# Kernel optimization log

Hardware: AMD Instinct MI355X
Metric: run time of the kernel (lower is better)

## Reference

```python
import jax, jax.numpy as jnp
import numpy as np

N_NODES = 100000
N_EDGES = 1600000
FEAT = 128


def setup_inputs() -> dict:
    key = jax.random.key(0)
    k_h, k_hin, k_src, k_dst, k_w, k_b = jax.random.split(key, 6)
    h = jax.random.normal(k_h, (N_NODES, FEAT), dtype=jnp.float32)
    h_in = jax.random.normal(k_hin, (N_NODES, FEAT), dtype=jnp.float32)
    src = jax.random.randint(k_src, (N_EDGES,), 0, N_NODES, dtype=jnp.int64)
    dst = jax.random.randint(k_dst, (N_EDGES,), 0, N_NODES, dtype=jnp.int64)
    W = jax.random.normal(k_w, (FEAT, FEAT), dtype=jnp.float32) / np.sqrt(FEAT)
    b = jax.random.normal(k_b, (FEAT,), dtype=jnp.float32) * 0.01
    return {"h": h, "h_in": h_in, "src": src, "dst": dst, "W": W, "b": b}


def reference(h, h_in, src, dst, W, b):
    # h_in is accepted but unused, matching the original forward signature.
    n = h.shape[0]
    hr = jax.nn.relu(h @ W.T + b)  # [N, d]
    # copy_src message + mean reduce over in-edges == segment mean by dst
    msg_sum = jax.ops.segment_sum(hr[src], dst, num_segments=n)  # [N, d]
    deg = jax.ops.segment_sum(jnp.ones(dst.shape, dtype=hr.dtype), dst, num_segments=n)  # [N]
    agg = msg_sum / jnp.maximum(deg, 1.0)[:, None]
    # DGL UDF reduce only overwrites nodes with in-degree > 0;
    # zero-in-degree nodes keep their pre-aggregation feature hr.
    return jnp.where(deg[:, None] > 0, agg, hr)
```

## Files before the change

kernel.cpp:

```cpp
#include <hip/hip_runtime.h>
#include <hip/hip_bf16.h>


#define FEAT 128
#define BM 64
#define NPB 256
#define CAP 6144

using bf16 = __hip_bfloat16;
typedef __attribute__((ext_vector_type(8))) short short8_;
typedef __attribute__((ext_vector_type(4))) short bhalf4;
typedef __attribute__((ext_vector_type(4))) float floatx4;

__device__ __forceinline__ bhalf4 cvt4(float4 f) {
    bhalf4 s;
    s[0] = __bfloat16_as_short(__float2bfloat16(f.x));
    s[1] = __bfloat16_as_short(__float2bfloat16(f.y));
    s[2] = __bfloat16_as_short(__float2bfloat16(f.z));
    s[3] = __bfloat16_as_short(__float2bfloat16(f.w));
    return s;
}
__device__ __forceinline__ float b2f(short s) {
    return __bfloat162float(__short_as_bfloat16(s));
}

__launch_bounds__(256)
__global__ void gemm_kernel(const float* __restrict__ h, const float* __restrict__ W,
                            const float* __restrict__ b, bf16* __restrict__ hr, int M) {
    __shared__ bf16 sA[BM][136];
    __shared__ bf16 sW[FEAT][136];

    const int tid  = threadIdx.x;
    const int row0 = blockIdx.x * BM;

    #pragma unroll
    for (int i = 0; i < 8; ++i) {
        int v = i * 256 + tid;
        int r = v >> 4;
        int c = (v & 15) * 8;
        const float4* wp = (const float4*)(W + (size_t)r * FEAT + c);
        bhalf4 lo = cvt4(wp[0]);
        bhalf4 hi = cvt4(wp[1]);
        short8_ s;
        s[0] = lo[0]; s[1] = lo[1]; s[2] = lo[2]; s[3] = lo[3];
        s[4] = hi[0]; s[5] = hi[1]; s[6] = hi[2]; s[7] = hi[3];
        *(short8_*)(&sW[r][c]) = s;
    }
    #pragma unroll
    for (int i = 0; i < 8; ++i) {
        int v = i * 256 + tid;
        int r = v >> 5;
        int c = (v & 31) * 4;
        int row = row0 + r;
        float4 f = make_float4(0.f, 0.f, 0.f, 0.f);
        if (row < M) f = *(const float4*)(h + (size_t)row * FEAT + c);
        *(bhalf4*)(&sA[r][c]) = cvt4(f);
    }
    __syncthreads();

    const int wave = tid >> 6;
    const int lane = tid & 63;
    const int m    = lane & 15;
    const int ko   = (lane >> 4) * 8;

    floatx4 acc[8];
    #pragma unroll
    for (int t = 0; t < 8; ++t) acc[t] = floatx4{0.f, 0.f, 0.f, 0.f};

    #pragma unroll
    for (int k0 = 0; k0 < FEAT; k0 += 32) {
        short8_ afrag = *(const short8_*)(&sA[wave * 16 + m][k0 + ko]);
        #pragma unroll
        for (int nt = 0; nt < 8; ++nt) {
            short8_ bfrag = *(const short8_*)(&sW[nt * 16 + m][k0 + ko]);
            acc[nt] = __builtin_amdgcn_mfma_f32_16x16x32_bf16(afrag, bfrag, acc[nt], 0, 0, 0);
        }
    }

    const int rbase = row0 + wave * 16 + (lane >> 4) * 4;
    #pragma unroll
    for (int nt = 0; nt < 8; ++nt) {
        int col = nt * 16 + m;
        float bias = b[col];
        #pragma unroll
        for (int r = 0; r < 4; ++r) {
            int row = rbase + r;
            if (row < M) {
                float v = fmaxf(acc[nt][r] + bias, 0.0f);
                hr[(size_t)row * FEAT + col] = __float2bfloat16(v);
            }
        }
    }
}

__launch_bounds__(512)
__global__ void bin_kernel(const int* __restrict__ src, const int* __restrict__ dst,
                           int* __restrict__ cursor, int* __restrict__ binned,
                           int E, int B) {
    __shared__ int cnt[512];
    __shared__ int resv[512];
    __shared__ int cur[512];
    int t = threadIdx.x;
    cnt[t] = 0; cur[t] = 0;
    __syncthreads();

    int v4 = blockIdx.x * 512 + t;
    int e0 = v4 * 4;
    int4 d = make_int4(0, 0, 0, 0), s = make_int4(0, 0, 0, 0);
    bool full = (e0 + 3 < E);
    if (full) {
        d = ((const int4*)dst)[v4];
        s = ((const int4*)src)[v4];
        atomicAdd(&cnt[d.x >> 8], 1);
        atomicAdd(&cnt[d.y >> 8], 1);
        atomicAdd(&cnt[d.z >> 8], 1);
        atomicAdd(&cnt[d.w >> 8], 1);
    } else {
        for (int j = 0; j < 4; ++j) {
            int e = e0 + j;
            if (e < E) atomicAdd(&cnt[dst[e] >> 8], 1);
        }
    }
    __syncthreads();
    if (t < B && cnt[t]) resv[t] = atomicAdd(&cursor[t], cnt[t]);
    __syncthreads();

    if (full) {
        int bk, r, pos;
        bk = d.x >> 8; r = atomicAdd(&cur[bk], 1); pos = resv[bk] + r;
        if (pos < CAP) binned[bk * CAP + pos] = s.x | ((d.x & (NPB - 1)) << 17);
        bk = d.y >> 8; r = atomicAdd(&cur[bk], 1); pos = resv[bk] + r;
        if (pos < CAP) binned[bk * CAP + pos] = s.y | ((d.y & (NPB - 1)) << 17);
        bk = d.z >> 8; r = atomicAdd(&cur[bk], 1); pos = resv[bk] + r;
        if (pos < CAP) binned[bk * CAP + pos] = s.z | ((d.z & (NPB - 1)) << 17);
        bk = d.w >> 8; r = atomicAdd(&cur[bk], 1); pos = resv[bk] + r;
        if (pos < CAP) binned[bk * CAP + pos] = s.w | ((d.w & (NPB - 1)) << 17);
    } else {
        for (int j = 0; j < 4; ++j) {
            int e = e0 + j;
            if (e < E) {
                int dd = dst[e];
                int bk = dd >> 8;
                int r = atomicAdd(&cur[bk], 1);
                int pos = resv[bk] + r;
                if (pos < CAP) binned[bk * CAP + pos] = src[e] | ((dd & (NPB - 1)) << 17);
            }
        }
    }
}

__launch_bounds__(512)
__global__ void bscan_kernel(const int* __restrict__ cursor, int* __restrict__ bbase, int B) {
    __shared__ int sd[512];
    int t = threadIdx.x;
    int v = (t < B) ? min(cursor[t], CAP) : 0;
    sd[t] = v;
    __syncthreads();
    for (int off = 1; off < 512; off <<= 1) {
        int y = (t >= off) ? sd[t - off] : 0;
        __syncthreads();
        sd[t] += y;
        __syncthreads();
    }
    if (t < B) bbase[t] = sd[t] - v;
    if (t == 511) bbase[B] = sd[511];
}

__launch_bounds__(512)
__global__ void build_kernel(const int* __restrict__ binned, const int* __restrict__ bbase,
                             int* __restrict__ rowptr, int* __restrict__ deg,
                             int* __restrict__ eidx, int N) {
    __shared__ int scnt[NPB];
    __shared__ int ssc[512];
    int t = threadIdx.x;
    int bk = blockIdx.x;
    if (t < NPB) scnt[t] = 0;
    __syncthreads();

    int base = bbase[bk];
    int cnt  = bbase[bk + 1] - base;
    const int* bp = binned + (size_t)bk * CAP;

    for (int i = t; i < cnt; i += 512) {
        atomicAdd(&scnt[(bp[i] >> 17) & (NPB - 1)], 1);
    }
    __syncthreads();

    int node = bk * NPB + t;
    int myc = (t < NPB) ? scnt[t] : 0;
    if (t < NPB && node < N) deg[node] = myc;

    ssc[t] = myc;
    __syncthreads();
    for (int off = 1; off < 512; off <<= 1) {
        int y = (t >= off) ? ssc[t - off] : 0;
        __syncthreads();
        ssc[t] += y;
        __syncthreads();
    }
    int excl = ssc[t] - myc;
    if (t < NPB) {
        if (node < N) rowptr[node] = base + excl;
        scnt[t] = excl;
    }
    __syncthreads();

    for (int i = t; i < cnt; i += 512) {
        int p  = bp[i];
        int ld = (p >> 17) & (NPB - 1);
        int slot = atomicAdd(&scnt[ld], 1);
        eidx[base + slot] = p & 0x1FFFF;
    }
}

__launch_bounds__(256)
__global__ void gather_kernel(const bf16* __restrict__ hr,
                              const int* __restrict__ rowptr,
                              const int* __restrict__ deg,
                              const int* __restrict__ eidx,
                              float* __restrict__ out, int N) {
    int node = blockIdx.x * 16 + (threadIdx.x >> 4);
    if (node >= N) return;
    int l16 = threadIdx.x & 15;

    int beg = rowptr[node];
    int d   = deg[node];
    int end = beg + d;

    const short8_* hp8 = (const short8_*)hr;

    float a0[8], a1[8], a2[8], a3[8];
    #pragma unroll
    for (int j = 0; j < 8; ++j) { a0[j] = 0.f; a1[j] = 0.f; a2[j] = 0.f; a3[j] = 0.f; }

    int e = beg;
    for (; e + 3 < end; e += 4) {
        int s0 = eidx[e + 0];
        int s1 = eidx[e + 1];
        int s2 = eidx[e + 2];
        int s3 = eidx[e + 3];
        short8_ v0 = hp8[(size_t)s0 * 16 + l16];
        short8_ v1 = hp8[(size_t)s1 * 16 + l16];
        short8_ v2 = hp8[(size_t)s2 * 16 + l16];
        short8_ v3 = hp8[(size_t)s3 * 16 + l16];
        #pragma unroll
        for (int j = 0; j < 8; ++j) a0[j] += b2f(v0[j]);
        #pragma unroll
        for (int j = 0; j < 8; ++j) a1[j] += b2f(v1[j]);
        #pragma unroll
        for (int j = 0; j < 8; ++j) a2[j] += b2f(v2[j]);
        #pragma unroll
        for (int j = 0; j < 8; ++j) a3[j] += b2f(v3[j]);
    }
    for (; e < end; ++e) {
        int s0 = eidx[e];
        short8_ v0 = hp8[(size_t)s0 * 16 + l16];
        #pragma unroll
        for (int j = 0; j < 8; ++j) a0[j] += b2f(v0[j]);
    }

    #pragma unroll
    for (int j = 0; j < 8; ++j) a0[j] += a1[j] + a2[j] + a3[j];

    float r[8];
    if (d > 0) {
        float inv = 1.0f / (float)d;
        #pragma unroll
        for (int j = 0; j < 8; ++j) r[j] = a0[j] * inv;
    } else {
        short8_ v = hp8[(size_t)node * 16 + l16];
        #pragma unroll
        for (int j = 0; j < 8; ++j) r[j] = b2f(v[j]);
    }

    float* op = out + (size_t)node * FEAT + l16 * 8;
    *(float4*)(op)     = make_float4(r[0], r[1], r[2], r[3]);
    *(float4*)(op + 4) = make_float4(r[4], r[5], r[6], r[7]);
}

extern "C" void kernel_launch(void* const* d_in, const int* in_sizes, int n_in,
                              void* d_out, int out_size, void* d_ws, size_t ws_size,
                              hipStream_t stream) {
    const float* h   = (const float*)d_in[0];
    const int*   src = (const int*)d_in[2];
    const int*   dst = (const int*)d_in[3];
    const float* W   = (const float*)d_in[4];
    const float* b   = (const float*)d_in[5];
    float* out = (float*)d_out;

    const int N = in_sizes[0] / FEAT;
    const int E = in_sizes[2];
    const int B = (N + NPB - 1) / NPB;

    char* ws = (char*)d_ws;
    size_t off = 0;
    bf16* hr     = (bf16*)(ws + off); off += (size_t)N * FEAT * 2;
    int*  rowptr = (int*)(ws + off);  off += (size_t)N * 4;
    int*  deg    = (int*)(ws + off);  off += (size_t)N * 4;
    int*  eidx   = (int*)(ws + off);  off += (size_t)E * 4;
    int*  cursor = (int*)(ws + off);  off += 512 * 4;
    int*  bbase  = (int*)(ws + off);  off += 513 * 4;

    int* binned = (int*)d_out;

    (void)hipMemsetAsync(cursor, 0, 512 * 4, stream);

    const int gb = (N + BM - 1) / BM;
    gemm_kernel<<<dim3(gb), dim3(256), 0, stream>>>(h, W, b, hr, N);

    const int nb = (E + 2047) / 2048;
    bin_kernel<<<dim3(nb), dim3(512), 0, stream>>>(src, dst, cursor, binned, E, B);

    bscan_kernel<<<dim3(1), dim3(512), 0, stream>>>(cursor, bbase, B);

    build_kernel<<<dim3(B), dim3(512), 0, stream>>>(binned, bbase, rowptr, deg, eidx, N);

    gather_kernel<<<dim3((N + 15) / 16), dim3(256), 0, stream>>>(hr, rowptr, deg, eidx, out, N);
}
```

Measured before the change: 264.2 us.

## Merge GEMM and edge binning into one launch; fold bucket scan into build

GEMM blocks and edge-binning blocks now share one grid, branching on block index, so the two independent stages run side by side. Each binning block handles 4096 edges with 256 threads instead of 2048 with 512. The separate single-block bucket-scan kernel is removed, and every build block redoes the 391-entry prefix scan of the cursors itself. This saves two launches and lets binning overlap the GEMM, at the cost of redundant scan work per block and a larger shared-memory footprint for the binning blocks.

```diff
diff --git a/kernel.cpp b/kernel.cpp
--- a/kernel.cpp
+++ b/kernel.cpp
@@ -25,12 +25,89 @@
 }
 
 __launch_bounds__(256)
-__global__ void gemm_kernel(const float* __restrict__ h, const float* __restrict__ W,
-                            const float* __restrict__ b, bf16* __restrict__ hr, int M) {
-    __shared__ bf16 sA[BM][136];
-    __shared__ bf16 sW[FEAT][136];
-
-    const int tid  = threadIdx.x;
+__global__ void fused_kernel(const float* __restrict__ h, const float* __restrict__ W,
+                             const float* __restrict__ b, bf16* __restrict__ hr, int M,
+                             const int* __restrict__ src, const int* __restrict__ dst,
+                             int* __restrict__ cursor, int* __restrict__ binned,
+                             int E, int B, int gb) {
+    __shared__ __align__(16) char smem[(BM + FEAT) * 136 * 2];
+    const int tid = threadIdx.x;
+
+    if (blockIdx.x >= gb) {
+        int* cnt  = (int*)smem;
+        int* resv = cnt + 512;
+        int* cur  = resv + 512;
+        cnt[tid] = 0; cnt[tid + 256] = 0;
+        cur[tid] = 0; cur[tid + 256] = 0;
+        __syncthreads();
+
+        const int bid = blockIdx.x - gb;
+        const int4* d4 = (const int4*)dst;
+        const int4* s4 = (const int4*)src;
+
+        int4 dv[4], sv[4];
+        bool fullv[4];
+        #pragma unroll
+        for (int i = 0; i < 4; ++i) {
+            int v4 = bid * 1024 + i * 256 + tid;
+            int e0 = v4 * 4;
+            fullv[i] = (e0 + 3 < E);
+            if (fullv[i]) {
+                dv[i] = d4[v4];
+                sv[i] = s4[v4];
+                atomicAdd(&cnt[dv[i].x >> 8], 1);
+                atomicAdd(&cnt[dv[i].y >> 8], 1);
+                atomicAdd(&cnt[dv[i].z >> 8], 1);
+                atomicAdd(&cnt[dv[i].w >> 8], 1);
+            } else {
+                dv[i] = make_int4(0, 0, 0, 0);
+                sv[i] = make_int4(0, 0, 0, 0);
+                for (int j = 0; j < 4; ++j) {
+                    int e = e0 + j;
+                    if (e < E) atomicAdd(&cnt[dst[e] >> 8], 1);
+                }
+            }
+        }
+        __syncthreads();
+        #pragma unroll
+        for (int q = 0; q < 2; ++q) {
+            int k = tid + q * 256;
+            if (k < B && cnt[k]) resv[k] = atomicAdd(&cursor[k], cnt[k]);
+        }
+        __syncthreads();
+
+        #pragma unroll
+        for (int i = 0; i < 4; ++i) {
+            int e0 = (bid * 1024 + i * 256 + tid) * 4;
+            if (fullv[i]) {
+                int bk, r, pos;
+                bk = dv[i].x >> 8; r = atomicAdd(&cur[bk], 1); pos = resv[bk] + r;
+                if (pos < CAP) binned[bk * CAP + pos] = sv[i].x | ((dv[i].x & (NPB - 1)) << 17);
+                bk = dv[i].y >> 8; r = atomicAdd(&cur[bk], 1); pos = resv[bk] + r;
+                if (pos < CAP) binned[bk * CAP + pos] = sv[i].y | ((dv[i].y & (NPB - 1)) << 17);
+                bk = dv[i].z >> 8; r = atomicAdd(&cur[bk], 1); pos = resv[bk] + r;
+                if (pos < CAP) binned[bk * CAP + pos] = sv[i].z | ((dv[i].z & (NPB - 1)) << 17);
+                bk = dv[i].w >> 8; r = atomicAdd(&cur[bk], 1); pos = resv[bk] + r;
+                if (pos < CAP) binned[bk * CAP + pos] = sv[i].w | ((dv[i].w & (NPB - 1)) << 17);
+            } else {
+                for (int j = 0; j < 4; ++j) {
+                    int e = e0 + j;
+                    if (e < E) {
+                        int dd = dst[e];
+                        int bk = dd >> 8;
+                        int r = atomicAdd(&cur[bk], 1);
+                        int pos = resv[bk] + r;
+                        if (pos < CAP) binned[bk * CAP + pos] = src[e] | ((dd & (NPB - 1)) << 17);
+                    }
+                }
+            }
+        }
+        return;
+    }
+
+    bf16 (*sA)[136] = (bf16(*)[136])smem;
+    bf16 (*sW)[136] = (bf16(*)[136])(smem + BM * 136 * 2);
+
     const int row0 = blockIdx.x * BM;
 
     #pragma unroll
@@ -94,91 +171,28 @@
 }
 
 __launch_bounds__(512)
-__global__ void bin_kernel(const int* __restrict__ src, const int* __restrict__ dst,
-                           int* __restrict__ cursor, int* __restrict__ binned,
-                           int E, int B) {
-    __shared__ int cnt[512];
-    __shared__ int resv[512];
-    __shared__ int cur[512];
-    int t = threadIdx.x;
-    cnt[t] = 0; cur[t] = 0;
-    __syncthreads();
-
-    int v4 = blockIdx.x * 512 + t;
-    int e0 = v4 * 4;
-    int4 d = make_int4(0, 0, 0, 0), s = make_int4(0, 0, 0, 0);
-    bool full = (e0 + 3 < E);
-    if (full) {
-        d = ((const int4*)dst)[v4];
-        s = ((const int4*)src)[v4];
-        atomicAdd(&cnt[d.x >> 8], 1);
-        atomicAdd(&cnt[d.y >> 8], 1);
-        atomicAdd(&cnt[d.z >> 8], 1);
-        atomicAdd(&cnt[d.w >> 8], 1);
-    } else {
-        for (int j = 0; j < 4; ++j) {
-            int e = e0 + j;
-            if (e < E) atomicAdd(&cnt[dst[e] >> 8], 1);
-        }
-    }
-    __syncthreads();
-    if (t < B && cnt[t]) resv[t] = atomicAdd(&cursor[t], cnt[t]);
-    __syncthreads();
-
-    if (full) {
-        int bk, r, pos;
-        bk = d.x >> 8; r = atomicAdd(&cur[bk], 1); pos = resv[bk] + r;
-        if (pos < CAP) binned[bk * CAP + pos] = s.x | ((d.x & (NPB - 1)) << 17);
-        bk = d.y >> 8; r = atomicAdd(&cur[bk], 1); pos = resv[bk] + r;
-        if (pos < CAP) binned[bk * CAP + pos] = s.y | ((d.y & (NPB - 1)) << 17);
-        bk = d.z >> 8; r = atomicAdd(&cur[bk], 1); pos = resv[bk] + r;
-        if (pos < CAP) binned[bk * CAP + pos] = s.z | ((d.z & (NPB - 1)) << 17);
-        bk = d.w >> 8; r = atomicAdd(&cur[bk], 1); pos = resv[bk] + r;
-        if (pos < CAP) binned[bk * CAP + pos] = s.w | ((d.w & (NPB - 1)) << 17);
-    } else {
-        for (int j = 0; j < 4; ++j) {
-            int e = e0 + j;
-            if (e < E) {
-                int dd = dst[e];
-                int bk = dd >> 8;
-                int r = atomicAdd(&cur[bk], 1);
-                int pos = resv[bk] + r;
-                if (pos < CAP) binned[bk * CAP + pos] = src[e] | ((dd & (NPB - 1)) << 17);
-            }
-        }
-    }
-}
-
-__launch_bounds__(512)
-__global__ void bscan_kernel(const int* __restrict__ cursor, int* __restrict__ bbase, int B) {
+__global__ void build_kernel(const int* __restrict__ binned, const int* __restrict__ cursor,
+                             int* __restrict__ rowptr, int* __restrict__ deg,
+                             int* __restrict__ eidx, int N, int B) {
     __shared__ int sd[512];
-    int t = threadIdx.x;
-    int v = (t < B) ? min(cursor[t], CAP) : 0;
-    sd[t] = v;
-    __syncthreads();
-    for (int off = 1; off < 512; off <<= 1) {
-        int y = (t >= off) ? sd[t - off] : 0;
-        __syncthreads();
-        sd[t] += y;
-        __syncthreads();
-    }
-    if (t < B) bbase[t] = sd[t] - v;
-    if (t == 511) bbase[B] = sd[511];
-}
-
-__launch_bounds__(512)
-__global__ void build_kernel(const int* __restrict__ binned, const int* __restrict__ bbase,
-                             int* __restrict__ rowptr, int* __restrict__ deg,
-                             int* __restrict__ eidx, int N) {
     __shared__ int scnt[NPB];
     __shared__ int ssc[512];
     int t = threadIdx.x;
     int bk = blockIdx.x;
+
+    int cv = (t < B) ? min(cursor[t], CAP) : 0;
+    sd[t] = cv;
     if (t < NPB) scnt[t] = 0;
     __syncthreads();
-
-    int base = bbase[bk];
-    int cnt  = bbase[bk + 1] - base;
+    for (int off = 1; off < 512; off <<= 1) {
+        int y = (t >= off) ? sd[t - off] : 0;
+        __syncthreads();
+        sd[t] += y;
+        __syncthreads();
+    }
+    int base = (bk > 0) ? sd[bk - 1] : 0;
+    int cnt  = sd[bk] - base;
+
     const int* bp = binned + (size_t)bk * CAP;
 
     for (int i = t; i < cnt; i += 512) {
@@ -299,21 +313,17 @@
     int*  deg    = (int*)(ws + off);  off += (size_t)N * 4;
     int*  eidx   = (int*)(ws + off);  off += (size_t)E * 4;
     int*  cursor = (int*)(ws + off);  off += 512 * 4;
-    int*  bbase  = (int*)(ws + off);  off += 513 * 4;
 
     int* binned = (int*)d_out;
 
     (void)hipMemsetAsync(cursor, 0, 512 * 4, stream);
 
     const int gb = (N + BM - 1) / BM;
-    gemm_kernel<<<dim3(gb), dim3(256), 0, stream>>>(h, W, b, hr, N);
-
-    const int nb = (E + 2047) / 2048;
-    bin_kernel<<<dim3(nb), dim3(512), 0, stream>>>(src, dst, cursor, binned, E, B);
-
-    bscan_kernel<<<dim3(1), dim3(512), 0, stream>>>(cursor, bbase, B);
-
-    build_kernel<<<dim3(B), dim3(512), 0, stream>>>(binned, bbase, rowptr, deg, eidx, N);
+    const int nb = (E + 4095) / 4096;
+    fused_kernel<<<dim3(gb + nb), dim3(256), 0, stream>>>(
+        h, W, b, hr, N, src, dst, cursor, binned, E, B, gb);
+
+    build_kernel<<<dim3(B), dim3(512), 0, stream>>>(binned, cursor, rowptr, deg, eidx, N, B);
 
     gather_kernel<<<dim3((N + 15) / 16), dim3(256), 0, stream>>>(hr, rowptr, deg, eidx, out, N);
 }
```

Measured after the change: 246.1 us. -6.8%, faster.
